# Kernel tuning notes

Measured on AMD Instinct MI355X. Metric: run time of the kernel, lower is better.

## Reference

```python
import jax, jax.numpy as jnp
import numpy as np
from jax import lax

# dims: batch, seq_len, d_model, heads, d_ff, num_scales, compression_ratio
B, L, D, H, F, S, CR = 4, 1024, 1024, 16, 4096, 4, 2


def setup_inputs() -> dict:
    key = jax.random.key(0)
    ks = jax.random.split(key, 12)
    def rn(k, shape, s=0.02):
        return jax.random.normal(k, shape, dtype=jnp.float32) * s
    return {
        'x': jax.random.normal(ks[0], (B, L, D), dtype=jnp.float32),
        'W_dc': rn(ks[1], (D, D, 3)),            # dilated conv kernel (OIH)
        'b_dc': jnp.zeros((D,), jnp.float32),
        'W_dec': rn(ks[2], (S - 1, D, D, CR)),    # strided decomposition convs
        'Wq': rn(ks[3], (S, D, D)),               # per-scale query proj
        'Wk': rn(ks[4], (S, D, D)),               # per-scale key proj
        'Wv': rn(ks[5], (D, D)),                  # shared value proj
        'Wo': rn(ks[6], (D, D)),                  # shared output proj
        'agg_logits': rn(ks[7], (S,), 1.0),       # convex aggregation logits
        'gamma1': jnp.ones((D,), jnp.float32), 'beta1': jnp.zeros((D,), jnp.float32),
        'gamma2': jnp.ones((D,), jnp.float32), 'beta2': jnp.zeros((D,), jnp.float32),
        'W1': rn(ks[8], (D, F)), 'b1': jnp.zeros((F,), jnp.float32),
        'W2': rn(ks[9], (F, D)), 'b2': jnp.zeros((D,), jnp.float32),
    }


def _conv1d(x_blc, w_oik, stride, pad, rdil):
    # x: [B, L, Cin] -> [B, L', Cout]; w: [Cout, Cin, K]
    y = lax.conv_general_dilated(
        x_blc.transpose(0, 2, 1), w_oik, (stride,), [(pad, pad)],
        rhs_dilation=(rdil,), dimension_numbers=('NCH', 'OIH', 'NCH'))
    return y.transpose(0, 2, 1)


def _ln(x, g, b, eps=1e-5):
    mu = x.mean(-1, keepdims=True)
    v = x.var(-1, keepdims=True)
    return (x - mu) * lax.rsqrt(v + eps) * g + b


def reference(x, W_dc, b_dc, W_dec, Wq, Wk, Wv, Wo, agg_logits,
              gamma1, beta1, gamma2, beta2, W1, b1, W2, b2):
    dh = D // H
    inv_sqrt_dh = 1.0 / jnp.sqrt(jnp.float32(dh))
    residual = x
    # 1. dilated conv (k=3, dil=2, pad=2 -> same length) + ReLU (dropout=eval/identity)
    xc = jax.nn.relu(_conv1d(x, W_dc, 1, 2, 2) + b_dc)
    # 2. hierarchical decomposition: strided convs halving seq length per scale
    scales = [xc]
    for s in range(S - 1):
        scales.append(_conv1d(scales[-1], W_dec[s], CR, 0, 1))
    # 3. multiscale attention: full-res queries attend to each compressed scale;
    #    value projection Wv shared across scales
    outs = []
    for s in range(S):
        Ls = scales[s].shape[1]
        q = (xc @ Wq[s]).reshape(B, L, H, dh)
        k = (scales[s] @ Wk[s]).reshape(B, Ls, H, dh)
        v = (scales[s] @ Wv).reshape(B, Ls, H, dh)
        att = jax.nn.softmax(jnp.einsum('bqhd,bkhd->bhqk', q, k) * inv_sqrt_dh, axis=-1)
        o = jnp.einsum('bhqk,bkhd->bqhd', att, v).reshape(B, L, D) @ Wo
        outs.append(o)
    # 4. convex (optimization-driven) aggregation + entropy sparsity aux loss
    w = jax.nn.softmax(agg_logits)
    maha = jnp.einsum('s,sbld->bld', w, jnp.stack(outs))
    aux_loss = -jnp.sum(w * jnp.log(w + 1e-9))
    # 5. residual + LN + FFN (exact GELU, as torch nn.GELU default)
    x1 = _ln(residual + maha, gamma1, beta1)
    ffn = jax.nn.gelu(x1 @ W1 + b1, approximate=False) @ W2 + b2
    out = _ln(x1 + ffn, gamma2, beta2)
    return out, aux_loss
```

## Files before the change

kernel.cpp:

```cpp
#include <hip/hip_runtime.h>
#include <cstddef>

#define DB 4
#define DL 1024
#define DD 1024
#define DH 16
#define DF 4096

typedef __attribute__((ext_vector_type(8))) short short8;
typedef __attribute__((ext_vector_type(4))) float float4v;

static __device__ __forceinline__ short f2bf(float f) {
    unsigned u = __float_as_uint(f);
    unsigned r = (u + 0x7FFFu + ((u >> 16) & 1u)) >> 16;
    return (short)r;
}

#define GLOAD_LDS16(gp, lp)                                                          \
    __builtin_amdgcn_global_load_lds(                                                \
        (const __attribute__((address_space(1))) void*)(gp),                         \
        (__attribute__((address_space(3))) void*)(lp), 16, 0, 0)

__global__ __launch_bounds__(256) void prep_all_kernel(
    const float* __restrict__ Wdc, const float* __restrict__ Wdec,
    const float* __restrict__ Wq, const float* __restrict__ Wk,
    const float* __restrict__ Wv, const float* __restrict__ Wo,
    const float* __restrict__ W1, const float* __restrict__ W2,
    const float* __restrict__ x, const float* __restrict__ agg,
    short* __restrict__ wdc_bt, short* __restrict__ wdec_bt,
    short* __restrict__ wq4t, short* __restrict__ wkvt, short* __restrict__ wot,
    short* __restrict__ w1t, short* __restrict__ w2t, short* __restrict__ xpad,
    float* __restrict__ wagg, float* __restrict__ aux) {
    __shared__ float tile[32][33];
    const size_t M1 = 1024 * 1024;
    int blk = blockIdx.x, tid = threadIdx.x;
    if (blk < 12288) {
        int idx = blk * 256 + tid;
        int i = idx & 1023, o = (idx >> 10) & 1023, k = idx >> 20;
        wdc_bt[idx] = f2bf(Wdc[((size_t)o * 1024 + i) * 3 + k]);
        return;
    }
    if (blk < 36864) {
        int idx = (blk - 12288) * 256 + tid;
        int i = idx & 1023, k2 = (idx >> 10) & 1, n = (idx >> 11) & 1023, s = idx >> 21;
        wdec_bt[idx] = f2bf(Wdec[(((size_t)(s * 1024 + n)) * 1024 + i) * 2 + k2]);
        return;
    }
    if (blk < 58368) {
        const float* src; short* dst; int K, N, bx, by;
        if (blk < 50176) {
            int r = blk - 36864;
            int z = r >> 10, rem = r & 1023;
            bx = rem & 31; by = rem >> 5; K = 1024; N = 1024;
            if (z < 4)      { src = Wq + (size_t)z * M1;       dst = wq4t + (size_t)z * M1; }
            else if (z < 8) { src = Wk + (size_t)(z - 4) * M1; dst = wkvt + (size_t)(z - 4) * 2 * M1; }
            else if (z < 12){ src = Wv;                        dst = wkvt + (size_t)(z - 8) * 2 * M1 + M1; }
            else            { src = Wo;                        dst = wot; }
        } else if (blk < 54272) {
            int r = blk - 50176;
            bx = r & 127; by = r >> 7; K = 1024; N = 4096; src = W1; dst = w1t;
        } else {
            int r = blk - 54272;
            bx = r & 31; by = r >> 5; K = 4096; N = 1024; src = W2; dst = w2t;
        }
        int n0 = bx << 5, k0 = by << 5;
        int cc = tid & 31, rr = tid >> 5;
#pragma unroll
        for (int p = 0; p < 4; p++) {
            int kk = (p << 3) + rr;
            tile[kk][cc] = src[(size_t)(k0 + kk) * N + n0 + cc];
        }
        __syncthreads();
#pragma unroll
        for (int p = 0; p < 4; p++) {
            int nn = (p << 3) + rr;
            dst[(size_t)(n0 + nn) * K + k0 + cc] = f2bf(tile[cc][nn]);
        }
        return;
    }
    if (blk < 74816) {
        int idx = (blk - 58368) * 256 + tid;
        int d = idx & 1023;
        int row = (idx >> 10) % 1028;
        int b = (idx >> 10) / 1028;
        int l = row - 2;
        float v = (l >= 0 && l < DL) ? x[((size_t)(b * DL + l)) * DD + d] : 0.f;
        xpad[idx] = f2bf(v);
        return;
    }
    if (tid == 0) {
        float l0 = agg[0], l1 = agg[1], l2 = agg[2], l3 = agg[3];
        float m = fmaxf(fmaxf(l0, l1), fmaxf(l2, l3));
        float e0 = __expf(l0 - m), e1 = __expf(l1 - m);
        float e2 = __expf(l2 - m), e3 = __expf(l3 - m);
        float ssum = e0 + e1 + e2 + e3;
        float w0 = e0 / ssum, w1 = e1 / ssum, w2 = e2 / ssum, w3 = e3 / ssum;
        wagg[0] = w0; wagg[1] = w1; wagg[2] = w2; wagg[3] = w3;
        *aux = -(w0 * logf(w0 + 1e-9f) + w1 * logf(w1 + 1e-9f) +
                 w2 * logf(w2 + 1e-9f) + w3 * logf(w3 + 1e-9f));
    }
}

template <int ACT, int OBF>
__global__ __launch_bounds__(256) void mgemm_kernel(
    const short* __restrict__ A, const short* __restrict__ Bt,
    const float* __restrict__ bias, void* __restrict__ Cv,
    int M, int N, int K) {
    __shared__ short As[2][128 * 32];
    __shared__ short Bs[2][128 * 32];
    int tid = threadIdx.x;
    int wave = tid >> 6, lane = tid & 63;
    int lq = lane & 15, quad = lane >> 4;
    int m0 = blockIdx.y << 7, n0 = blockIdx.x << 7;
    int wm = (wave & 1) << 6, wn = (wave >> 1) << 6;
    int r0 = tid >> 2, r1 = (256 + tid) >> 2;
    int kc0 = (tid & 3) << 3;
    const short* Ag0 = A + (size_t)(m0 + r0) * K + kc0;
    const short* Ag1 = A + (size_t)(m0 + r1) * K + kc0;
    const short* Bg0 = Bt + (size_t)(n0 + r0) * K + kc0;
    const short* Bg1 = Bt + (size_t)(n0 + r1) * K + kc0;
    float4v acc[4][4];
#pragma unroll
    for (int mi = 0; mi < 4; mi++)
#pragma unroll
        for (int ni = 0; ni < 4; ni++) acc[mi][ni] = (float4v){0.f, 0.f, 0.f, 0.f};

#define MG_STAGE(BUF, KO)                                                \
    {                                                                    \
        GLOAD_LDS16(Ag0 + (KO), As[BUF] + tid * 8);                      \
        GLOAD_LDS16(Ag1 + (KO), As[BUF] + (256 + tid) * 8);              \
        GLOAD_LDS16(Bg0 + (KO), Bs[BUF] + tid * 8);                      \
        GLOAD_LDS16(Bg1 + (KO), Bs[BUF] + (256 + tid) * 8);              \
    }
    int nk = K >> 5;
    MG_STAGE(0, 0);
    __syncthreads();
    for (int t = 0; t < nk; t++) {
        int cur = t & 1;
        if (t + 1 < nk) MG_STAGE(cur ^ 1, (t + 1) << 5);
        short8 af[4], bfr[4];
#pragma unroll
        for (int mi = 0; mi < 4; mi++)
            af[mi] = *(const short8*)(As[cur] + ((wm + (mi << 4) + lq) << 5) + (quad << 3));
#pragma unroll
        for (int ni = 0; ni < 4; ni++)
            bfr[ni] = *(const short8*)(Bs[cur] + ((wn + (ni << 4) + lq) << 5) + (quad << 3));
#pragma unroll
        for (int mi = 0; mi < 4; mi++)
#pragma unroll
            for (int ni = 0; ni < 4; ni++)
                acc[mi][ni] = __builtin_amdgcn_mfma_f32_16x16x32_bf16(
                    af[mi], bfr[ni], acc[mi][ni], 0, 0, 0);
        __syncthreads();
    }
#undef MG_STAGE
#pragma unroll
    for (int ni = 0; ni < 4; ni++) {
        int col = n0 + wn + (ni << 4) + lq;
        float bv = bias ? bias[col] : 0.f;
#pragma unroll
        for (int mi = 0; mi < 4; mi++) {
#pragma unroll
            for (int r = 0; r < 4; r++) {
                int row = m0 + wm + (mi << 4) + (quad << 2) + r;
                float v = acc[mi][ni][r] + bv;
                if (ACT == 1) v = 0.5f * v * (1.0f + erff(v * 0.70710678118654752f));
                if (OBF) ((short*)Cv)[(size_t)row * N + col] = f2bf(v);
                else ((float*)Cv)[(size_t)row * N + col] = v;
            }
        }
    }
}

__global__ __launch_bounds__(256) void kvgemm_kernel(
    const short* __restrict__ acts, const short* __restrict__ wkvt,
    short* __restrict__ kvall, short* __restrict__ kfrall) {
    __shared__ short As[2][128 * 32];
    __shared__ short Bs[2][128 * 32];
    int my = blockIdx.y;
    int s = my < 32 ? 0 : my < 48 ? 1 : my < 56 ? 2 : 3;
    int m0 = my << 7;
    int rb = s == 0 ? 0 : s == 1 ? 4096 : s == 2 ? 6144 : 7168;
    size_t doff = s == 0 ? 0 : s == 1 ? 4194304 : s == 2 ? 6291456 : 7340032;
    int Ls = DL >> s;
    const short* Bt = wkvt + (size_t)s * 2097152;
    const int K = 1024, N = 2048;
    int tid = threadIdx.x;
    int wave = tid >> 6, lane = tid & 63;
    int lq = lane & 15, quad = lane >> 4;
    int n0 = blockIdx.x << 7;
    int wm = (wave & 1) << 6, wn = (wave >> 1) << 6;
    int r0 = tid >> 2, r1 = (256 + tid) >> 2;
    int kc0 = (tid & 3) << 3;
    const short* Ag0 = acts + (size_t)(m0 + r0) * K + kc0;
    const short* Ag1 = acts + (size_t)(m0 + r1) * K + kc0;
    const short* Bg0 = Bt + (size_t)(n0 + r0) * K + kc0;
    const short* Bg1 = Bt + (size_t)(n0 + r1) * K + kc0;
    float4v acc[4][4];
#pragma unroll
    for (int mi = 0; mi < 4; mi++)
#pragma unroll
        for (int ni = 0; ni < 4; ni++) acc[mi][ni] = (float4v){0.f, 0.f, 0.f, 0.f};

#define KV_STAGE(BUF, KO)                                                \
    {                                                                    \
        GLOAD_LDS16(Ag0 + (KO), As[BUF] + tid * 8);                      \
        GLOAD_LDS16(Ag1 + (KO), As[BUF] + (256 + tid) * 8);              \
        GLOAD_LDS16(Bg0 + (KO), Bs[BUF] + tid * 8);                      \
        GLOAD_LDS16(Bg1 + (KO), Bs[BUF] + (256 + tid) * 8);              \
    }
    int nk = K >> 5;
    KV_STAGE(0, 0);
    __syncthreads();
    for (int t = 0; t < nk; t++) {
        int cur = t & 1;
        if (t + 1 < nk) KV_STAGE(cur ^ 1, (t + 1) << 5);
        short8 af[4], bfr[4];
#pragma unroll
        for (int mi = 0; mi < 4; mi++)
            af[mi] = *(const short8*)(As[cur] + ((wm + (mi << 4) + lq) << 5) + (quad << 3));
#pragma unroll
        for (int ni = 0; ni < 4; ni++)
            bfr[ni] = *(const short8*)(Bs[cur] + ((wn + (ni << 4) + lq) << 5) + (quad << 3));
#pragma unroll
        for (int mi = 0; mi < 4; mi++)
#pragma unroll
            for (int ni = 0; ni < 4; ni++)
                acc[mi][ni] = __builtin_amdgcn_mfma_f32_16x16x32_bf16(
                    af[mi], bfr[ni], acc[mi][ni], 0, 0, 0);
        __syncthreads();
    }
#undef KV_STAGE
    bool isK = (n0 < 1024);
#pragma unroll
    for (int ni = 0; ni < 4; ni++) {
        int col = n0 + wn + (ni << 4) + lq;
        if (isK) {
            int h = col >> 6, dc = (col >> 3) & 7, di = col & 7;
#pragma unroll
            for (int mi = 0; mi < 4; mi++)
#pragma unroll
                for (int r = 0; r < 4; r++) {
                    int row = m0 + wm + (mi << 4) + (quad << 2) + r;
                    int jg = row - rb;
                    int b = jg >> (10 - s);
                    int j = jg & (Ls - 1);
                    int bh = (b << 4) | h;
                    size_t addr = doff + (((size_t)bh * (Ls >> 4) + (j >> 4)) << 10) +
                                  (dc << 7) + ((j & 15) << 3) + di;
                    kfrall[addr] = f2bf(acc[mi][ni][r]);
                }
        } else {
#pragma unroll
            for (int mi = 0; mi < 4; mi++)
#pragma unroll
                for (int r = 0; r < 4; r++) {
                    int row = m0 + wm + (mi << 4) + (quad << 2) + r;
                    kvall[(size_t)row * N + col] = f2bf(acc[mi][ni][r]);
                }
        }
    }
}

__global__ __launch_bounds__(256) void mgemm_pk_kernel(
    const short* __restrict__ A, const short* __restrict__ Bt,
    const float* __restrict__ bias, float* __restrict__ Cout,
    int M, int N, int Kfull, int KH) {
    __shared__ short As[2][128 * 32];
    __shared__ short Bs[2][128 * 32];
    int kz = blockIdx.z;
    const short* Ab = A + (size_t)kz * KH;
    const short* Btb = Bt + (size_t)kz * KH;
    float* Co = Cout + (size_t)kz * M * N;
    int tid = threadIdx.x;
    int wave = tid >> 6, lane = tid & 63;
    int lq = lane & 15, quad = lane >> 4;
    int m0 = blockIdx.y << 7, n0 = blockIdx.x << 7;
    int wm = (wave & 1) << 6, wn = (wave >> 1) << 6;
    int r0 = tid >> 2, r1 = (256 + tid) >> 2;
    int kc0 = (tid & 3) << 3;
    const short* Ag0 = Ab + (size_t)(m0 + r0) * Kfull + kc0;
    const short* Ag1 = Ab + (size_t)(m0 + r1) * Kfull + kc0;
    const short* Bg0 = Btb + (size_t)(n0 + r0) * Kfull + kc0;
    const short* Bg1 = Btb + (size_t)(n0 + r1) * Kfull + kc0;
    float4v acc[4][4];
#pragma unroll
    for (int mi = 0; mi < 4; mi++)
#pragma unroll
        for (int ni = 0; ni < 4; ni++) acc[mi][ni] = (float4v){0.f, 0.f, 0.f, 0.f};

#define PK_STAGE(BUF, KO)                                                \
    {                                                                    \
        GLOAD_LDS16(Ag0 + (KO), As[BUF] + tid * 8);                      \
        GLOAD_LDS16(Ag1 + (KO), As[BUF] + (256 + tid) * 8);              \
        GLOAD_LDS16(Bg0 + (KO), Bs[BUF] + tid * 8);                      \
        GLOAD_LDS16(Bg1 + (KO), Bs[BUF] + (256 + tid) * 8);              \
    }
    int nk = KH >> 5;
    PK_STAGE(0, 0);
    __syncthreads();
    for (int t = 0; t < nk; t++) {
        int cur = t & 1;
        if (t + 1 < nk) PK_STAGE(cur ^ 1, (t + 1) << 5);
        short8 af[4], bfr[4];
#pragma unroll
        for (int mi = 0; mi < 4; mi++)
            af[mi] = *(const short8*)(As[cur] + ((wm + (mi << 4) + lq) << 5) + (quad << 3));
#pragma unroll
        for (int ni = 0; ni < 4; ni++)
            bfr[ni] = *(const short8*)(Bs[cur] + ((wn + (ni << 4) + lq) << 5) + (quad << 3));
#pragma unroll
        for (int mi = 0; mi < 4; mi++)
#pragma unroll
            for (int ni = 0; ni < 4; ni++)
                acc[mi][ni] = __builtin_amdgcn_mfma_f32_16x16x32_bf16(
                    af[mi], bfr[ni], acc[mi][ni], 0, 0, 0);
        __syncthreads();
    }
#undef PK_STAGE
#pragma unroll
    for (int ni = 0; ni < 4; ni++) {
        int col = n0 + wn + (ni << 4) + lq;
        float bv = (bias && kz == 0) ? bias[col] : 0.f;
#pragma unroll
        for (int mi = 0; mi < 4; mi++)
#pragma unroll
            for (int r = 0; r < 4; r++) {
                int row = m0 + wm + (mi << 4) + (quad << 2) + r;
                __builtin_nontemporal_store(acc[mi][ni][r] + bv,
                                            &Co[(size_t)row * N + col]);
            }
    }
}

__global__ __launch_bounds__(256) void sumcast4_kernel(
    const float* __restrict__ p, size_t stride, short* __restrict__ outp) {
    int idx = (blockIdx.x * 256 + threadIdx.x) << 2;
    float4v a0 = __builtin_nontemporal_load((const float4v*)&p[idx]);
    float4v a1 = __builtin_nontemporal_load((const float4v*)&p[stride + idx]);
    float4v a2 = __builtin_nontemporal_load((const float4v*)&p[2 * stride + idx]);
    float4v a3 = __builtin_nontemporal_load((const float4v*)&p[3 * stride + idx]);
    ushort4 u;
    u.x = (unsigned short)f2bf(a0[0] + a1[0] + a2[0] + a3[0]);
    u.y = (unsigned short)f2bf(a0[1] + a1[1] + a2[1] + a3[1]);
    u.z = (unsigned short)f2bf(a0[2] + a1[2] + a2[2] + a3[2]);
    u.w = (unsigned short)f2bf(a0[3] + a1[3] + a2[3] + a3[3]);
    *(ushort4*)&outp[idx] = u;
}

__global__ __launch_bounds__(256) void convdil_pk_kernel(
    const short* __restrict__ xp, const short* __restrict__ Wt,
    float* __restrict__ pbuf) {
    __shared__ short As[2][128 * 32];
    __shared__ short Bs[2][128 * 32];
    int kp = blockIdx.z;
    int tid = threadIdx.x;
    int wave = tid >> 6, lane = tid & 63;
    int lq = lane & 15, quad = lane >> 4;
    int m0 = blockIdx.y << 7, n0 = blockIdx.x << 7;
    int wm = (wave & 1) << 6, wn = (wave >> 1) << 6;
    int b = m0 >> 10, ll0 = m0 & 1023;
    int r0 = tid >> 2, r1 = (256 + tid) >> 2;
    int kc = (tid & 3) << 3;
    float* Co = pbuf + (size_t)kp * DB * DL * DD;
    const short* Abase = xp + ((size_t)(b * 1028 + ll0 + 2 * kp)) * DD + kc;
    const short* Bbase = Wt + (size_t)kp * DD * DD;
    const short* Bg0 = Bbase + (size_t)(n0 + r0) * DD + kc;
    const short* Bg1 = Bbase + (size_t)(n0 + r1) * DD + kc;
    float4v acc[4][4];
#pragma unroll
    for (int mi = 0; mi < 4; mi++)
#pragma unroll
        for (int ni = 0; ni < 4; ni++) acc[mi][ni] = (float4v){0.f, 0.f, 0.f, 0.f};

#define CD_STAGE(BUF, KO)                                                        \
    {                                                                            \
        GLOAD_LDS16(Abase + (size_t)r0 * DD + (KO), As[BUF] + tid * 8);          \
        GLOAD_LDS16(Abase + (size_t)r1 * DD + (KO), As[BUF] + (256 + tid) * 8);  \
        GLOAD_LDS16(Bg0 + (KO), Bs[BUF] + tid * 8);                              \
        GLOAD_LDS16(Bg1 + (KO), Bs[BUF] + (256 + tid) * 8);                      \
    }
    int nk = DD >> 5;
    CD_STAGE(0, 0);
    __syncthreads();
    for (int t = 0; t < nk; t++) {
        int cur = t & 1;
        if (t + 1 < nk) CD_STAGE(cur ^ 1, (t + 1) << 5);
        short8 af[4], bfr[4];
#pragma unroll
        for (int mi = 0; mi < 4; mi++)
            af[mi] = *(const short8*)(As[cur] + ((wm + (mi << 4) + lq) << 5) + (quad << 3));
#pragma unroll
        for (int ni = 0; ni < 4; ni++)
            bfr[ni] = *(const short8*)(Bs[cur] + ((wn + (ni << 4) + lq) << 5) + (quad << 3));
#pragma unroll
        for (int mi = 0; mi < 4; mi++)
#pragma unroll
            for (int ni = 0; ni < 4; ni++)
                acc[mi][ni] = __builtin_amdgcn_mfma_f32_16x16x32_bf16(
                    af[mi], bfr[ni], acc[mi][ni], 0, 0, 0);
        __syncthreads();
    }
#undef CD_STAGE
#pragma unroll
    for (int ni = 0; ni < 4; ni++) {
        int col = n0 + wn + (ni << 4) + lq;
#pragma unroll
        for (int mi = 0; mi < 4; mi++)
#pragma unroll
            for (int r = 0; r < 4; r++) {
                int row = m0 + wm + (mi << 4) + (quad << 2) + r;
                __builtin_nontemporal_store(acc[mi][ni][r],
                                            &Co[(size_t)row * DD + col]);
            }
    }
}

__global__ __launch_bounds__(256) void convcomb_kernel(
    const float* __restrict__ pbuf, const float* __restrict__ bvec,
    short* __restrict__ xcb) {
    const size_t M4 = (size_t)DB * DL * DD;
    int idx = (blockIdx.x * 256 + threadIdx.x) << 2;
    int col = idx & 1023;
    float4v p0 = __builtin_nontemporal_load((const float4v*)&pbuf[idx]);
    float4v p1 = __builtin_nontemporal_load((const float4v*)&pbuf[M4 + idx]);
    float4v p2 = __builtin_nontemporal_load((const float4v*)&pbuf[2 * M4 + idx]);
    float4v bb = *(const float4v*)&bvec[col];
    ushort4 u;
    u.x = (unsigned short)f2bf(fmaxf(p0[0] + p1[0] + p2[0] + bb[0], 0.f));
    u.y = (unsigned short)f2bf(fmaxf(p0[1] + p1[1] + p2[1] + bb[1], 0.f));
    u.z = (unsigned short)f2bf(fmaxf(p0[2] + p1[2] + p2[2] + bb[2], 0.f));
    u.w = (unsigned short)f2bf(fmaxf(p0[3] + p1[3] + p2[3] + bb[3], 0.f));
    *(ushort4*)&xcb[idx] = u;
}

__global__ __launch_bounds__(256) void vfrag_all_kernel(const short* __restrict__ kvall,
                                                        short* __restrict__ vfr0) {
    __shared__ short tile[32][33];
    int flat = blockIdx.x;
    int s, base, rb;
    size_t doff;
    if (flat < 4096)      { s = 0; base = 0;    rb = 0;    doff = 0; }
    else if (flat < 6144) { s = 1; base = 4096; rb = 4096; doff = 4194304; }
    else if (flat < 7168) { s = 2; base = 6144; rb = 6144; doff = 6291456; }
    else                  { s = 3; base = 7168; rb = 7168; doff = 7340032; }
    int rem = flat - base;
    int Ls = DL >> s;
    int nt = Ls >> 5;
    int j0t = rem & (nt - 1);
    int rest = rem >> (5 - s);
    int dt = rest & 1;
    int bh = rest >> 1;
    int j0 = j0t << 5, d0 = dt << 5;
    int b = bh >> 4, h = bh & 15;
    int tid = threadIdx.x;
    int cc = tid & 31, rr = tid >> 5;
#pragma unroll
    for (int p = 0; p < 4; p++) {
        int jj = (p << 3) + rr;
        tile[jj][cc] = kvall[((size_t)(rb + b * Ls + j0 + jj) << 11) + 1024 +
                             (h << 6) + d0 + cc];
    }
    __syncthreads();
    int c = j0 >> 6, ks = (j0 >> 5) & 1;
    int pc = (((cc >> 2) & 1) << 4) | ((cc >> 3) << 2) | (cc & 3);
#pragma unroll
    for (int p = 0; p < 4; p++) {
        int d = d0 + (p << 3) + rr;
        int tt = d >> 4, lqv = d & 15;
        size_t off = doff + (((size_t)bh * (Ls >> 6) + c) << 12) + (ks << 11) +
                     (tt << 9) + ((cc & 24) << 4) + (lqv << 3) + (cc & 7);
        vfr0[off] = tile[pc][(p << 3) + rr];
    }
}

static __device__ __forceinline__ float fexp2(float x) {
    return __builtin_amdgcn_exp2f(x);
}

#define STAGE9(BUF, TILE)                                                         \
    {                                                                             \
        const short* _gs = (w < 2)                                                \
            ? kt + ((size_t)(TILE) << 12) + (w << 11) + (lane << 3)               \
            : vt + ((size_t)(TILE) << 12) + ((w - 2) << 11) + (lane << 3);        \
        short* _lb = sbuf[BUF] + (w << 11) + (lane << 3);                         \
        _Pragma("unroll") for (int _i = 0; _i < 4; _i++)                          \
            GLOAD_LDS16(_gs + (_i << 9), _lb + (_i << 9));                        \
    }

__global__ __launch_bounds__(256) void attn_fused9_kernel(
    const short* __restrict__ qb4, const short* __restrict__ kfr0,
    const short* __restrict__ vfr0, const float* __restrict__ wagg,
    short* __restrict__ attb) {
    __shared__ __align__(16) short sbuf[2][8192];
    int tid = threadIdx.x;
    int w = tid >> 6, lane = tid & 63;
    int lq = lane & 15, quad = lane >> 4;
    int bh = blockIdx.x;
    int b = bh >> 4, h = bh & 15;
    int qrow0 = b * DL + (blockIdx.y << 6) + (w << 4);
    const float c_exp = 0.18033688f;
    int fo = (quad << 7) + (lq << 3);

    float fin[4][4];
#pragma unroll
    for (int t = 0; t < 4; t++)
#pragma unroll
        for (int r = 0; r < 4; r++) fin[t][r] = 0.f;

#pragma unroll 1
    for (int s = 0; s < 4; s++) {
        int Ls = DL >> s;
        size_t doff = s == 0 ? 0 : s == 1 ? 4194304 : s == 2 ? 6291456 : 7340032;

        const short* qbase = qb4 + ((size_t)(qrow0 + lq) << 12) + (s << 10) +
                             (h << 6) + (quad << 3);
        short8 qf0 = __builtin_nontemporal_load((const short8*)qbase);
        short8 qf1 = __builtin_nontemporal_load((const short8*)(qbase + 32));

        const short* kt = kfr0 + doff + (((size_t)bh * (Ls >> 4)) << 10);
        const short* vt = vfr0 + doff + (((size_t)bh * (Ls >> 6)) << 12);

        float4v O[4];
        float lsum = 0.f;
#pragma unroll
        for (int t = 0; t < 4; t++) O[t] = (float4v){0.f, 0.f, 0.f, 0.f};

        int nt = Ls >> 6;
        STAGE9(0, 0);
#pragma unroll 1
        for (int c = 0; c < nt; c++) {
            __syncthreads();
            int cur = c & 1;
            if (c + 1 < nt) STAGE9(cur ^ 1, c + 1);
            const short* kl = sbuf[cur] + fo;
            const short* vl = sbuf[cur] + 4096 + fo;

            float4v S[4];
#pragma unroll
            for (int t = 0; t < 4; t++) {
                short8 kf0 = *(const short8*)(kl + (t << 10));
                short8 kf1 = *(const short8*)(kl + (t << 10) + 512);
                float4v zz = (float4v){0.f, 0.f, 0.f, 0.f};
                zz = __builtin_amdgcn_mfma_f32_16x16x32_bf16(kf0, qf0, zz, 0, 0, 0);
                S[t] = __builtin_amdgcn_mfma_f32_16x16x32_bf16(kf1, qf1, zz, 0, 0, 0);
            }

            unsigned wpk[8];
#pragma unroll
            for (int t = 0; t < 4; t++) {
                float p0 = fexp2(S[t][0] * c_exp);
                float p1 = fexp2(S[t][1] * c_exp);
                float p2 = fexp2(S[t][2] * c_exp);
                float p3 = fexp2(S[t][3] * c_exp);
                lsum += p0 + p1 + p2 + p3;
                wpk[2 * t]     = (__float_as_uint(p1) & 0xFFFF0000u) |
                                 (__float_as_uint(p0) >> 16);
                wpk[2 * t + 1] = (__float_as_uint(p3) & 0xFFFF0000u) |
                                 (__float_as_uint(p2) >> 16);
            }
            union AFU { unsigned u[4]; short8 s8; };
            AFU af0, af1;
            af0.u[0] = wpk[0]; af0.u[1] = wpk[1]; af0.u[2] = wpk[2]; af0.u[3] = wpk[3];
            af1.u[0] = wpk[4]; af1.u[1] = wpk[5]; af1.u[2] = wpk[6]; af1.u[3] = wpk[7];
#pragma unroll
            for (int t = 0; t < 4; t++) {
                short8 vf = *(const short8*)(vl + (t << 9));
                O[t] = __builtin_amdgcn_mfma_f32_16x16x32_bf16(af0.s8, vf, O[t], 0, 0, 0);
            }
#pragma unroll
            for (int t = 0; t < 4; t++) {
                short8 vf = *(const short8*)(vl + 2048 + (t << 9));
                O[t] = __builtin_amdgcn_mfma_f32_16x16x32_bf16(af1.s8, vf, O[t], 0, 0, 0);
            }
        }
        __syncthreads();

        lsum += __shfl_xor(lsum, 16, 64);
        lsum += __shfl_xor(lsum, 32, 64);
        float wsc = wagg[s];
#pragma unroll
        for (int r = 0; r < 4; r++) {
            int sl = (lane & 48) | (((lane >> 4) << 2) + r);
            float lr = __shfl(lsum, sl, 64);
            float linv = wsc / lr;
#pragma unroll
            for (int t = 0; t < 4; t++) fin[t][r] += O[t][r] * linv;
        }
    }
#pragma unroll
    for (int r = 0; r < 4; r++) {
        size_t rbase = ((size_t)(qrow0 + (quad << 2) + r) << 10) + (h << 6) + lq;
#pragma unroll
        for (int t = 0; t < 4; t++)
            attb[rbase + (t << 4)] = f2bf(fin[t][r]);
    }
}

template <int NP, int OBF>
__global__ __launch_bounds__(256) void addlnN_kernel(
    const float* __restrict__ a, const float* __restrict__ pb, size_t pstride,
    const float* __restrict__ gam, const float* __restrict__ bet,
    float* __restrict__ out, short* __restrict__ outb) {
    __shared__ float redA[4], redB[4];
    int row = blockIdx.x, tid = threadIdx.x;
    size_t base = (size_t)row * DD + (tid << 2);
    float4v av = *(const float4v*)&a[base];
    float s0 = av[0], s1 = av[1], s2 = av[2], s3 = av[3];
#pragma unroll
    for (int j = 0; j < NP; j++) {
        float4v pv = __builtin_nontemporal_load(
            (const float4v*)&pb[(size_t)j * pstride + base]);
        s0 += pv[0]; s1 += pv[1]; s2 += pv[2]; s3 += pv[3];
    }
    float lsum = s0 + s1 + s2 + s3;
    float lsq = s0 * s0 + s1 * s1 + s2 * s2 + s3 * s3;
#pragma unroll
    for (int o = 32; o > 0; o >>= 1) {
        lsum += __shfl_down(lsum, o, 64);
        lsq += __shfl_down(lsq, o, 64);
    }
    int lane = tid & 63, wid = tid >> 6;
    if (lane == 0) { redA[wid] = lsum; redB[wid] = lsq; }
    __syncthreads();
    float tsum = redA[0] + redA[1] + redA[2] + redA[3];
    float tsq = redB[0] + redB[1] + redB[2] + redB[3];
    float mean = tsum * (1.0f / DD);
    float var = tsq * (1.0f / DD) - mean * mean;
    float rstd = rsqrtf(var + 1e-5f);
    float4v gv = *(const float4v*)&gam[tid << 2];
    float4v bev = *(const float4v*)&bet[tid << 2];
    float4v o;
    o[0] = (s0 - mean) * rstd * gv[0] + bev[0];
    o[1] = (s1 - mean) * rstd * gv[1] + bev[1];
    o[2] = (s2 - mean) * rstd * gv[2] + bev[2];
    o[3] = (s3 - mean) * rstd * gv[3] + bev[3];
    *(float4v*)&out[base] = o;
    if (OBF) {
        ushort4 u;
        u.x = (unsigned short)f2bf(o[0]);
        u.y = (unsigned short)f2bf(o[1]);
        u.z = (unsigned short)f2bf(o[2]);
        u.w = (unsigned short)f2bf(o[3]);
        *(ushort4*)&outb[base] = u;
    }
}

extern "C" void kernel_launch(void* const* d_in, const int* in_sizes, int n_in,
                              void* d_out, int out_size, void* d_ws, size_t ws_size,
                              hipStream_t stream) {
    (void)in_sizes; (void)n_in; (void)out_size; (void)ws_size;
    const float* x   = (const float*)d_in[0];
    const float* Wdc = (const float*)d_in[1];
    const float* bdc = (const float*)d_in[2];
    const float* Wdec= (const float*)d_in[3];
    const float* Wq  = (const float*)d_in[4];
    const float* Wk  = (const float*)d_in[5];
    const float* Wv  = (const float*)d_in[6];
    const float* Wo  = (const float*)d_in[7];
    const float* agg = (const float*)d_in[8];
    const float* g1  = (const float*)d_in[9];
    const float* be1 = (const float*)d_in[10];
    const float* g2  = (const float*)d_in[11];
    const float* be2 = (const float*)d_in[12];
    const float* W1  = (const float*)d_in[13];
    const float* b1  = (const float*)d_in[14];
    const float* W2  = (const float*)d_in[15];
    const float* b2  = (const float*)d_in[16];
    float* out = (float*)d_out;

    float* ws = (float*)d_ws;
    size_t off = 0;
    auto alloc = [&](size_t nfloats) { float* p = ws + off; off += nfloats; return p; };
    const size_t M1 = 1024 * 1024;
    short* wdc_bt  = (short*)alloc(3 * M1 / 2);
    short* wdec_bt = (short*)alloc(3 * M1);
    short* wq4t    = (short*)alloc(2 * M1);
    short* wkvt    = (short*)alloc(4 * M1);
    short* wot     = (short*)alloc(M1 / 2);
    short* w1t     = (short*)alloc(2 * M1);
    short* w2t     = (short*)alloc(2 * M1);
    float* wagg    = alloc(64);
    short* xpad    = (short*)alloc(2105344);
    short* xcb     = (short*)alloc(2 * M1);
    short* s1b     = (short*)alloc(M1);
    short* s2b     = (short*)alloc(M1 / 2);
    short* s3b     = (short*)alloc(M1 / 4);
    short* qb4     = (short*)alloc(8 * M1);
    short* kvall   = (short*)alloc(7 * M1 + M1 / 2);
    short* kfrall  = (short*)alloc(3 * M1 + 3 * M1 / 4);
    short* vfrall  = (short*)alloc(3 * M1 + 3 * M1 / 4);
    short* attb    = (short*)alloc(2 * M1);
    float* x1      = alloc(4 * M1);
    short* x1b     = (short*)alloc(2 * M1);
    float* pkbuf   = alloc(8 * M1);
    short* hb      = qb4;
    float* convp   = (float*)qb4;
    float* pk4     = (float*)kvall;

    dim3 blk(256);
    prep_all_kernel<<<dim3(74817), blk, 0, stream>>>(
        Wdc, Wdec, Wq, Wk, Wv, Wo, W1, W2, x, agg,
        wdc_bt, wdec_bt, wq4t, wkvt, wot, w1t, w2t, xpad, wagg,
        out + (size_t)DB * DL * DD);

    convdil_pk_kernel<<<dim3(DD / 128, DB * DL / 128, 3), blk, 0, stream>>>(
        xpad, wdc_bt, convp);
    convcomb_kernel<<<dim3(4 * M1 / (256 * 4)), blk, 0, stream>>>(convp, bdc, xcb);

    mgemm_pk_kernel<<<dim3(8, 16, 4), blk, 0, stream>>>(
        xcb, wdec_bt, nullptr, pkbuf, 2048, DD, 2 * DD, 512);
    sumcast4_kernel<<<dim3(2 * M1 / 1024), blk, 0, stream>>>(pkbuf, 2 * M1, s1b);
    mgemm_pk_kernel<<<dim3(8, 8, 4), blk, 0, stream>>>(
        s1b, wdec_bt + 2 * M1, nullptr, pkbuf, 1024, DD, 2 * DD, 512);
    sumcast4_kernel<<<dim3(M1 / 1024), blk, 0, stream>>>(pkbuf, M1, s2b);
    mgemm_pk_kernel<<<dim3(8, 4, 4), blk, 0, stream>>>(
        s2b, wdec_bt + 4 * M1, nullptr, pkbuf, 512, DD, 2 * DD, 512);
    sumcast4_kernel<<<dim3(M1 / 2048), blk, 0, stream>>>(pkbuf, M1 / 2, s3b);

    mgemm_kernel<0, 1><<<dim3(32, 32), blk, 0, stream>>>(
        xcb, wq4t, nullptr, qb4, DB * DL, 4 * DD, DD);

    kvgemm_kernel<<<dim3(16, 60), blk, 0, stream>>>(xcb, wkvt, kvall, kfrall);

    vfrag_all_kernel<<<dim3(7680), blk, 0, stream>>>(kvall, vfrall);

    attn_fused9_kernel<<<dim3(DB * DH, DL / 64), blk, 0, stream>>>(
        qb4, kfrall, vfrall, wagg, attb);

    mgemm_pk_kernel<<<dim3(8, 32, 2), blk, 0, stream>>>(
        attb, wot, nullptr, pkbuf, DB * DL, DD, DD, DD / 2);

    addlnN_kernel<2, 1><<<dim3(DB * DL), blk, 0, stream>>>(
        x, pkbuf, 4 * M1, g1, be1, x1, x1b);

    mgemm_kernel<1, 1><<<dim3(DF / 128, (DB * DL) / 128), blk, 0, stream>>>(
        x1b, w1t, b1, hb, DB * DL, DF, DD);
    mgemm_pk_kernel<<<dim3(8, 32, 4), blk, 0, stream>>>(
        hb, w2t, b2, pk4, DB * DL, DD, DF, DF / 4);

    addlnN_kernel<4, 0><<<dim3(DB * DL), blk, 0, stream>>>(
        x1, pk4, 4 * M1, g2, be2, out, nullptr);
}
```

Before: 666.1 us.

## Triple-buffer GEMM LDS staging with partial vmcnt waits and XCD-aware tile remap

Four MFMA GEMM kernels move from double to triple LDS buffers and prefetch two k-steps ahead. The full __syncthreads is replaced with an s_waitcnt vmcnt(4) plus barrier, so one stage of global->LDS loads can stay in flight while the current tile is computed. The generic mgemm kernel also remaps block IDs so neighbouring tiles land on the same XCD, aiming for better L2 reuse. This raises LDS use per block, which may lower occupancy, and the remap hardcodes a 32-wide grid layout.

```diff
diff --git a/kernel.cpp b/kernel.cpp
--- a/kernel.cpp
+++ b/kernel.cpp
@@ -20,6 +20,17 @@
     __builtin_amdgcn_global_load_lds(                                                \
         (const __attribute__((address_space(1))) void*)(gp),                         \
         (__attribute__((address_space(3))) void*)(lp), 16, 0, 0)
+
+#define BAR_VM4()                                                        \
+    {                                                                    \
+        asm volatile("s_waitcnt vmcnt(4) lgkmcnt(0)" ::: "memory");      \
+        __builtin_amdgcn_s_barrier();                                    \
+    }
+#define BAR_VM0()                                                        \
+    {                                                                    \
+        asm volatile("s_waitcnt vmcnt(0) lgkmcnt(0)" ::: "memory");      \
+        __builtin_amdgcn_s_barrier();                                    \
+    }
 
 __global__ __launch_bounds__(256) void prep_all_kernel(
     const float* __restrict__ Wdc, const float* __restrict__ Wdec,
@@ -106,12 +117,16 @@
     const short* __restrict__ A, const short* __restrict__ Bt,
     const float* __restrict__ bias, void* __restrict__ Cv,
     int M, int N, int K) {
-    __shared__ short As[2][128 * 32];
-    __shared__ short Bs[2][128 * 32];
+    __shared__ short As[3][128 * 32];
+    __shared__ short Bs[3][128 * 32];
     int tid = threadIdx.x;
     int wave = tid >> 6, lane = tid & 63;
     int lq = lane & 15, quad = lane >> 4;
-    int m0 = blockIdx.y << 7, n0 = blockIdx.x << 7;
+    int lid = blockIdx.x + (blockIdx.y << 5);
+    int xcd = lid & 7, loc = lid >> 3;
+    int bx = ((xcd & 1) << 4) + (loc & 15);
+    int by = ((xcd >> 1) << 3) + (loc >> 4);
+    int m0 = by << 7, n0 = bx << 7;
     int wm = (wave & 1) << 6, wn = (wave >> 1) << 6;
     int r0 = tid >> 2, r1 = (256 + tid) >> 2;
     int kc0 = (tid & 3) << 3;
@@ -127,31 +142,33 @@
 
 #define MG_STAGE(BUF, KO)                                                \
     {                                                                    \
-        GLOAD_LDS16(Ag0 + (KO), As[BUF] + tid * 8);                      \
-        GLOAD_LDS16(Ag1 + (KO), As[BUF] + (256 + tid) * 8);              \
-        GLOAD_LDS16(Bg0 + (KO), Bs[BUF] + tid * 8);                      \
-        GLOAD_LDS16(Bg1 + (KO), Bs[BUF] + (256 + tid) * 8);              \
+        GLOAD_LDS16(Ag0 + (KO), &As[BUF][0] + tid * 8);                  \
+        GLOAD_LDS16(Ag1 + (KO), &As[BUF][0] + (256 + tid) * 8);          \
+        GLOAD_LDS16(Bg0 + (KO), &Bs[BUF][0] + tid * 8);                  \
+        GLOAD_LDS16(Bg1 + (KO), &Bs[BUF][0] + (256 + tid) * 8);          \
     }
     int nk = K >> 5;
     MG_STAGE(0, 0);
-    __syncthreads();
+    MG_STAGE(1, 32);
+    asm volatile("s_waitcnt vmcnt(4)" ::: "memory");
+    __builtin_amdgcn_s_barrier();
     for (int t = 0; t < nk; t++) {
-        int cur = t & 1;
-        if (t + 1 < nk) MG_STAGE(cur ^ 1, (t + 1) << 5);
+        int cur = t % 3;
+        if (t + 2 < nk) { int nb = (t + 2) % 3; MG_STAGE(nb, (t + 2) << 5); }
         short8 af[4], bfr[4];
 #pragma unroll
         for (int mi = 0; mi < 4; mi++)
-            af[mi] = *(const short8*)(As[cur] + ((wm + (mi << 4) + lq) << 5) + (quad << 3));
+            af[mi] = *(const short8*)(&As[cur][0] + ((wm + (mi << 4) + lq) << 5) + (quad << 3));
 #pragma unroll
         for (int ni = 0; ni < 4; ni++)
-            bfr[ni] = *(const short8*)(Bs[cur] + ((wn + (ni << 4) + lq) << 5) + (quad << 3));
+            bfr[ni] = *(const short8*)(&Bs[cur][0] + ((wn + (ni << 4) + lq) << 5) + (quad << 3));
 #pragma unroll
         for (int mi = 0; mi < 4; mi++)
 #pragma unroll
             for (int ni = 0; ni < 4; ni++)
                 acc[mi][ni] = __builtin_amdgcn_mfma_f32_16x16x32_bf16(
                     af[mi], bfr[ni], acc[mi][ni], 0, 0, 0);
-        __syncthreads();
+        if (t + 2 < nk) BAR_VM4() else BAR_VM0()
     }
 #undef MG_STAGE
 #pragma unroll
@@ -175,8 +192,8 @@
 __global__ __launch_bounds__(256) void kvgemm_kernel(
     const short* __restrict__ acts, const short* __restrict__ wkvt,
     short* __restrict__ kvall, short* __restrict__ kfrall) {
-    __shared__ short As[2][128 * 32];
-    __shared__ short Bs[2][128 * 32];
+    __shared__ short As[3][128 * 32];
+    __shared__ short Bs[3][128 * 32];
     int my = blockIdx.y;
     int s = my < 32 ? 0 : my < 48 ? 1 : my < 56 ? 2 : 3;
     int m0 = my << 7;
@@ -204,31 +221,33 @@
 
 #define KV_STAGE(BUF, KO)                                                \
     {                                                                    \
-        GLOAD_LDS16(Ag0 + (KO), As[BUF] + tid * 8);                      \
-        GLOAD_LDS16(Ag1 + (KO), As[BUF] + (256 + tid) * 8);              \
-        GLOAD_LDS16(Bg0 + (KO), Bs[BUF] + tid * 8);                      \
-        GLOAD_LDS16(Bg1 + (KO), Bs[BUF] + (256 + tid) * 8);              \
+        GLOAD_LDS16(Ag0 + (KO), &As[BUF][0] + tid * 8);                  \
+        GLOAD_LDS16(Ag1 + (KO), &As[BUF][0] + (256 + tid) * 8);          \
+        GLOAD_LDS16(Bg0 + (KO), &Bs[BUF][0] + tid * 8);                  \
+        GLOAD_LDS16(Bg1 + (KO), &Bs[BUF][0] + (256 + tid) * 8);          \
     }
     int nk = K >> 5;
     KV_STAGE(0, 0);
-    __syncthreads();
+    KV_STAGE(1, 32);
+    asm volatile("s_waitcnt vmcnt(4)" ::: "memory");
+    __builtin_amdgcn_s_barrier();
     for (int t = 0; t < nk; t++) {
-        int cur = t & 1;
-        if (t + 1 < nk) KV_STAGE(cur ^ 1, (t + 1) << 5);
+        int cur = t % 3;
+        if (t + 2 < nk) { int nb = (t + 2) % 3; KV_STAGE(nb, (t + 2) << 5); }
         short8 af[4], bfr[4];
 #pragma unroll
         for (int mi = 0; mi < 4; mi++)
-            af[mi] = *(const short8*)(As[cur] + ((wm + (mi << 4) + lq) << 5) + (quad << 3));
+            af[mi] = *(const short8*)(&As[cur][0] + ((wm + (mi << 4) + lq) << 5) + (quad << 3));
 #pragma unroll
         for (int ni = 0; ni < 4; ni++)
-            bfr[ni] = *(const short8*)(Bs[cur] + ((wn + (ni << 4) + lq) << 5) + (quad << 3));
+            bfr[ni] = *(const short8*)(&Bs[cur][0] + ((wn + (ni << 4) + lq) << 5) + (quad << 3));
 #pragma unroll
         for (int mi = 0; mi < 4; mi++)
 #pragma unroll
             for (int ni = 0; ni < 4; ni++)
                 acc[mi][ni] = __builtin_amdgcn_mfma_f32_16x16x32_bf16(
                     af[mi], bfr[ni], acc[mi][ni], 0, 0, 0);
-        __syncthreads();
+        if (t + 2 < nk) BAR_VM4() else BAR_VM0()
     }
 #undef KV_STAGE
     bool isK = (n0 < 1024);
@@ -266,8 +285,8 @@
     const short* __restrict__ A, const short* __restrict__ Bt,
     const float* __restrict__ bias, float* __restrict__ Cout,
     int M, int N, int Kfull, int KH) {
-    __shared__ short As[2][128 * 32];
-    __shared__ short Bs[2][128 * 32];
+    __shared__ short As[3][128 * 32];
+    __shared__ short Bs[3][128 * 32];
     int kz = blockIdx.z;
     const short* Ab = A + (size_t)kz * KH;
     const short* Btb = Bt + (size_t)kz * KH;
@@ -291,31 +310,33 @@
 
 #define PK_STAGE(BUF, KO)                                                \
     {                                                                    \
-        GLOAD_LDS16(Ag0 + (KO), As[BUF] + tid * 8);                      \
-        GLOAD_LDS16(Ag1 + (KO), As[BUF] + (256 + tid) * 8);              \
-        GLOAD_LDS16(Bg0 + (KO), Bs[BUF] + tid * 8);                      \
-        GLOAD_LDS16(Bg1 + (KO), Bs[BUF] + (256 + tid) * 8);              \
+        GLOAD_LDS16(Ag0 + (KO), &As[BUF][0] + tid * 8);                  \
+        GLOAD_LDS16(Ag1 + (KO), &As[BUF][0] + (256 + tid) * 8);          \
+        GLOAD_LDS16(Bg0 + (KO), &Bs[BUF][0] + tid * 8);                  \
+        GLOAD_LDS16(Bg1 + (KO), &Bs[BUF][0] + (256 + tid) * 8);          \
     }
     int nk = KH >> 5;
     PK_STAGE(0, 0);
-    __syncthreads();
+    PK_STAGE(1, 32);
+    asm volatile("s_waitcnt vmcnt(4)" ::: "memory");
+    __builtin_amdgcn_s_barrier();
     for (int t = 0; t < nk; t++) {
-        int cur = t & 1;
-        if (t + 1 < nk) PK_STAGE(cur ^ 1, (t + 1) << 5);
+        int cur = t % 3;
+        if (t + 2 < nk) { int nb = (t + 2) % 3; PK_STAGE(nb, (t + 2) << 5); }
         short8 af[4], bfr[4];
 #pragma unroll
         for (int mi = 0; mi < 4; mi++)
-            af[mi] = *(const short8*)(As[cur] + ((wm + (mi << 4) + lq) << 5) + (quad << 3));
+            af[mi] = *(const short8*)(&As[cur][0] + ((wm + (mi << 4) + lq) << 5) + (quad << 3));
 #pragma unroll
         for (int ni = 0; ni < 4; ni++)
-            bfr[ni] = *(const short8*)(Bs[cur] + ((wn + (ni << 4) + lq) << 5) + (quad << 3));
+            bfr[ni] = *(const short8*)(&Bs[cur][0] + ((wn + (ni << 4) + lq) << 5) + (quad << 3));
 #pragma unroll
         for (int mi = 0; mi < 4; mi++)
 #pragma unroll
             for (int ni = 0; ni < 4; ni++)
                 acc[mi][ni] = __builtin_amdgcn_mfma_f32_16x16x32_bf16(
                     af[mi], bfr[ni], acc[mi][ni], 0, 0, 0);
-        __syncthreads();
+        if (t + 2 < nk) BAR_VM4() else BAR_VM0()
     }
 #undef PK_STAGE
 #pragma unroll
@@ -351,8 +372,8 @@
 __global__ __launch_bounds__(256) void convdil_pk_kernel(
     const short* __restrict__ xp, const short* __restrict__ Wt,
     float* __restrict__ pbuf) {
-    __shared__ short As[2][128 * 32];
-    __shared__ short Bs[2][128 * 32];
+    __shared__ short As[3][128 * 32];
+    __shared__ short Bs[3][128 * 32];
     int kp = blockIdx.z;
     int tid = threadIdx.x;
     int wave = tid >> 6, lane = tid & 63;
@@ -375,31 +396,33 @@
 
 #define CD_STAGE(BUF, KO)                                                        \
     {                                                                            \
-        GLOAD_LDS16(Abase + (size_t)r0 * DD + (KO), As[BUF] + tid * 8);          \
-        GLOAD_LDS16(Abase + (size_t)r1 * DD + (KO), As[BUF] + (256 + tid) * 8);  \
-        GLOAD_LDS16(Bg0 + (KO), Bs[BUF] + tid * 8);                              \
-        GLOAD_LDS16(Bg1 + (KO), Bs[BUF] + (256 + tid) * 8);                      \
+        GLOAD_LDS16(Abase + (size_t)r0 * DD + (KO), &As[BUF][0] + tid * 8);      \
+        GLOAD_LDS16(Abase + (size_t)r1 * DD + (KO), &As[BUF][0] + (256 + tid) * 8); \
+        GLOAD_LDS16(Bg0 + (KO), &Bs[BUF][0] + tid * 8);                          \
+        GLOAD_LDS16(Bg1 + (KO), &Bs[BUF][0] + (256 + tid) * 8);                  \
     }
     int nk = DD >> 5;
     CD_STAGE(0, 0);
-    __syncthreads();
+    CD_STAGE(1, 32);
+    asm volatile("s_waitcnt vmcnt(4)" ::: "memory");
+    __builtin_amdgcn_s_barrier();
     for (int t = 0; t < nk; t++) {
-        int cur = t & 1;
-        if (t + 1 < nk) CD_STAGE(cur ^ 1, (t + 1) << 5);
+        int cur = t % 3;
+        if (t + 2 < nk) { int nb = (t + 2) % 3; CD_STAGE(nb, (t + 2) << 5); }
         short8 af[4], bfr[4];
 #pragma unroll
         for (int mi = 0; mi < 4; mi++)
-            af[mi] = *(const short8*)(As[cur] + ((wm + (mi << 4) + lq) << 5) + (quad << 3));
+            af[mi] = *(const short8*)(&As[cur][0] + ((wm + (mi << 4) + lq) << 5) + (quad << 3));
 #pragma unroll
         for (int ni = 0; ni < 4; ni++)
-            bfr[ni] = *(const short8*)(Bs[cur] + ((wn + (ni << 4) + lq) << 5) + (quad << 3));
+            bfr[ni] = *(const short8*)(&Bs[cur][0] + ((wn + (ni << 4) + lq) << 5) + (quad << 3));
 #pragma unroll
         for (int mi = 0; mi < 4; mi++)
 #pragma unroll
             for (int ni = 0; ni < 4; ni++)
                 acc[mi][ni] = __builtin_amdgcn_mfma_f32_16x16x32_bf16(
                     af[mi], bfr[ni], acc[mi][ni], 0, 0, 0);
-        __syncthreads();
+        if (t + 2 < nk) BAR_VM4() else BAR_VM0()
     }
 #undef CD_STAGE
 #pragma unroll
```

Result: no change. 667.1 us (+0.2%).
